# Optimization experiments

Measured on AMD Instinct MI355X. Metric: run time of the kernel, lower is better.

Reference implementation:

```python
import jax, jax.numpy as jnp
import numpy as np

B, T, D, H, L = 64, 512, 1024, 1024, 2


def _make_params(key, in_size, hidden):
    # 4 input-to-hidden and 4 hidden-to-hidden matrices, gate order (i, f, n, o),
    # concatenated along the output axis -> one GEMM per source per step.
    k1, k2 = jax.random.split(key)
    sx = (6.0 / (in_size + hidden)) ** 0.5   # xavier_uniform bound
    sh = (6.0 / (hidden + hidden)) ** 0.5
    Wx = jax.random.uniform(k1, (in_size, 4 * hidden), minval=-sx, maxval=sx, dtype=jnp.float32)
    Wh = jax.random.uniform(k2, (hidden, 4 * hidden), minval=-sh, maxval=sh, dtype=jnp.float32)
    b = jnp.zeros((4 * hidden,), dtype=jnp.float32)
    return Wx, Wh, b


def setup_inputs() -> dict:
    key = jax.random.key(0)
    kx, k0, k1 = jax.random.split(key, 3)
    x = jax.random.normal(kx, (B, T, D), dtype=jnp.float32)
    h0 = jnp.zeros((L, B, H), dtype=jnp.float32)
    c0 = jnp.zeros((L, B, H), dtype=jnp.float32)
    Wx0, Wh0, b0 = _make_params(k0, D, H)
    Wx1, Wh1, b1 = _make_params(k1, H, H)
    return {"x": x, "h0": h0, "c0": c0,
            "Wx0": Wx0, "Wh0": Wh0, "b0": b0,
            "Wx1": Wx1, "Wh1": Wh1, "b1": b1}


def _run_layer(xseq, h, c, Wx, Wh, b):
    # xseq: [T, B, in], h/c: [B, H]
    def step(carry, xt):
        h, c = carry
        g = xt @ Wx + h @ Wh + b                       # [B, 4H]
        i_t, f_t, n_t, o_t = jnp.split(g, 4, axis=-1)
        i_t = jax.nn.sigmoid(i_t)
        f_t = jax.nn.sigmoid(f_t)
        n_t = jnp.tanh(n_t)
        o_t = jax.nn.sigmoid(o_t)
        c = f_t * c + i_t * n_t
        h = o_t * jnp.tanh(c)
        return (h, c), h
    (h, c), ys = jax.lax.scan(step, (h, c), xseq)
    return ys, h, c                                     # ys: [T, B, H]


def reference(x, h0, c0, Wx0, Wh0, b0, Wx1, Wh1, b1):
    xs = jnp.transpose(x, (1, 0, 2))                    # [T, B, D]
    params = [(Wx0, Wh0, b0), (Wx1, Wh1, b1)]
    hs, cs = [], []
    for layer in range(L):
        Wx, Wh, b = params[layer]
        xs, h, c = _run_layer(xs, h0[layer], c0[layer], Wx, Wh, b)
        hs.append(h)
        cs.append(c)
    outputs = jnp.transpose(xs, (1, 0, 2))              # [B, T, H]
    return outputs, (jnp.stack(hs, 0), jnp.stack(cs, 0))
```

## Files before the change

kernel.cpp:

```cpp
#include <hip/hip_runtime.h>


#define NBLK 256
#define TPB  512
#define T_   512
#define HS_OFF 33554432
#define CS_OFF 33685504

typedef float  f32x4  __attribute__((ext_vector_type(4)));
typedef short  bf16x8 __attribute__((ext_vector_type(8)));

#define WS_CTR  0u
#define WS_W    69632u
#define WS_BIAS 33624064u
#define WS_XB   33656832u
#define WS_H0   100765696u
#define WS_H1   101027840u
#define WS_MIN  101289984u

__device__ __forceinline__ unsigned short f2bf(float f) {
  union { float f; unsigned u; } v; v.f = f;
  return (unsigned short)((v.u + 0x7FFFu + ((v.u >> 16) & 1u)) >> 16);
}
__device__ __forceinline__ float fsig(float x) { return 1.0f / (1.0f + __expf(-x)); }
__device__ __forceinline__ float ftanh(float x) {
  x = fminf(15.0f, fmaxf(-15.0f, x));
  float e = __expf(2.0f * x);
  return (e - 1.0f) / (e + 1.0f);
}

__global__ void kw(const float* __restrict__ Wx0, const float* __restrict__ Wh0,
                   const float* __restrict__ Wx1, const float* __restrict__ Wh1,
                   unsigned short* __restrict__ wp) {
  __shared__ float tile[64][65];
  int tb = blockIdx.x;
  int m  = tb >> 10;
  int kt = (tb >> 6) & 15;
  int nt = tb & 63;
  const float* W = (m == 0) ? Wx0 : (m == 1) ? Wh0 : (m == 2) ? Wx1 : Wh1;
  unsigned short* O = wp + (size_t)m * 4194304u;
  int k0 = kt * 64, n0 = nt * 64;
  int tx = threadIdx.x & 63, tg = threadIdx.x >> 6;
  for (int r = tg; r < 64; r += 4)
    tile[r][tx] = W[(size_t)(k0 + r) * 4096 + n0 + tx];
  __syncthreads();
  for (int r = tg; r < 64; r += 4) {
    int n = n0 + r;
    int p = ((n & 1023) << 2) | (n >> 10);
    O[(size_t)p * 1024 + k0 + tx] = f2bf(tile[tx][r]);
  }
}

__global__ void kx(const float* __restrict__ x, unsigned short* __restrict__ xb) {
  int row = blockIdx.x;
  int t = row >> 6, b = row & 63;
  const float4* src = (const float4*)(x + ((size_t)b * 512 + t) * 1024);
  float4 f = src[threadIdx.x];
  ushort4 o; o.x = f2bf(f.x); o.y = f2bf(f.y); o.z = f2bf(f.z); o.w = f2bf(f.w);
  ((ushort4*)(xb + (size_t)row * 1024))[threadIdx.x] = o;
}

__global__ void kmisc(const float* __restrict__ b0, const float* __restrict__ b1,
                      const float* __restrict__ h0in,
                      float* __restrict__ biasP,
                      unsigned short* __restrict__ h0r, unsigned short* __restrict__ h1r) {
  int idx = blockIdx.x * 256 + threadIdx.x;
  if (idx < 8192) {
    int layer = idx >> 12, p = idx & 4095;
    int orig = (p & 3) * 1024 + (p >> 2);
    biasP[idx] = (layer ? b1 : b0)[orig];
  } else if (idx < 139264) {
    int e = idx - 8192;
    int layer = e >> 16, o = e & 65535;
    int row = o >> 10, col = o & 1023;
    unsigned short v = f2bf(h0in[layer * 65536 + o]);
    int dst = 65536 + (col >> 3) * 512 + row * 8 + (col & 7);
    if (layer) h1r[dst] = v; else h0r[dst] = v;
  }
}

__global__ void __launch_bounds__(TPB)
klstm(const float* __restrict__ c0_in,
      const unsigned short* __restrict__ wp,
      const float* __restrict__ biasP,
      const unsigned short* __restrict__ xb,
      unsigned short* __restrict__ h0ring,
      unsigned short* __restrict__ h1ring,
      unsigned* __restrict__ ctrbase,
      float* __restrict__ out) {
  extern __shared__ char smem[];
  float* red  = (float*)(smem + 65536);
  float* lhb  = (float*)(smem + 73728);
  float* xred = (float*)(smem + 75776);
  unsigned* gctr  = ctrbase;
  unsigned* rctr  = ctrbase + 8192;
  unsigned* gflag = ctrbase + 9216;
  const int tid = threadIdx.x;
  const int w   = tid >> 6;
  const int l   = tid & 63;
  const int bid = blockIdx.x;
  const int n0  = bid * 16;
  const int layer = w >> 2;
  const int rbase = (w & 3) * 16;
  const int khalf = (w >> 2) * 512;
  const int grp   = bid >> 5;
  float* lh = lhb + w * 64;

  for (int m = 0; m < 4; m += 2) {
    const char* src = (const char*)(wp + (size_t)m * 4194304u + (size_t)n0 * 1024u);
    char* dst = smem + (m >> 1) * 32768;
    for (int i = tid; i < 2048; i += TPB) {
      int sb = i << 4;
      int c  = sb >> 11;
      int kb = sb & 2047;
      *(uint4*)(dst + (c << 11) + (kb ^ ((c & 7) << 4))) = *(const uint4*)(src + sb);
    }
  }

  bf16x8 wh0f[16], wh1f[16];
  {
    const unsigned short* p0 = wp + 4194304u + (size_t)(n0 + (l & 15)) * 1024u + khalf + (l >> 4) * 8;
    const unsigned short* p1 = wp + 3u * 4194304u + (size_t)(n0 + (l & 15)) * 1024u + khalf + (l >> 4) * 8;
    #pragma unroll
    for (int ks = 0; ks < 16; ++ks) {
      wh0f[ks] = *(const bf16x8*)(p0 + ks * 32);
      wh1f[ks] = *(const bf16x8*)(p1 + ks * 32);
    }
  }

  const int jg = bid * 4 + ((l & 15) >> 2);
  const float biasv = biasP[layer * 4096 + n0 + (l & 15)];
  const int qb = l & ~3;

  float cr[4];
  #pragma unroll
  for (int v = 0; v < 4; ++v)
    cr[v] = c0_in[layer * 65536 + (rbase + (l >> 4) * 4 + v) * 1024 + jg];

  const int ae0  = (rbase + (l & 15)) * 1024 + khalf + (l >> 4) * 8;
  const int hbase = ((khalf >> 3) + (l >> 4)) * 512 + (rbase + (l & 15)) * 8;
  const int lb0  = (l & 15) << 11;
  const int kb2  = khalf * 2 + (l >> 4) * 16;
  const int swz  = (l & 7) << 4;
  const int hsto = (bid >> 1) * 512 + 4 * (bid & 1);

  __syncthreads();

  f32x4 xacc = {0.f, 0.f, 0.f, 0.f};
  {
    #pragma unroll
    for (int kk = 0; kk < 16; ++kk) {
      bf16x8 ax = *(const bf16x8*)(xb + ae0 + kk * 32);
      bf16x8 b  = *(const bf16x8*)(smem + lb0 + ((kb2 + kk * 64) ^ swz));
      xacc = __builtin_amdgcn_mfma_f32_16x16x32_bf16(ax, b, xacc, 0, 0, 0);
    }
    if (w >= 4) {
      float* xr = xred + (size_t)(w & 3) * 256 + (size_t)l * 4;
      #pragma unroll
      for (int v = 0; v < 4; ++v) xr[v] = xacc[v];
    }
  }
  __syncthreads();

  for (int k = 0; k <= T_; ++k) {
    #pragma unroll
    for (int ks = 0; ks < 16; ++ks) {
      asm volatile("" :: "v"(wh0f[ks]));
      asm volatile("" :: "v"(wh1f[ks]));
    }

    const unsigned short* h0p = h0ring + ((k + 1) & 1) * 65536;
    const unsigned short* h1p = h1ring + (k & 1) * 65536;

    f32x4 acc0  = {0.f, 0.f, 0.f, 0.f};
    f32x4 acc1a = {0.f, 0.f, 0.f, 0.f};
    f32x4 acc1b = {0.f, 0.f, 0.f, 0.f};
    #pragma unroll
    for (int kk = 0; kk < 16; ++kk) {
      bf16x8 ah0 = *(const bf16x8*)(h0p + hbase + kk * 2048);
      bf16x8 ah1 = *(const bf16x8*)(h1p + hbase + kk * 2048);
      bf16x8 bx1 = *(const bf16x8*)(smem + 32768 + lb0 + ((kb2 + kk * 64) ^ swz));
      acc0  = __builtin_amdgcn_mfma_f32_16x16x32_bf16(ah0, wh0f[kk], acc0, 0, 0, 0);
      acc1a = __builtin_amdgcn_mfma_f32_16x16x32_bf16(ah0, bx1, acc1a, 0, 0, 0);
      acc1b = __builtin_amdgcn_mfma_f32_16x16x32_bf16(ah1, wh1f[kk], acc1b, 0, 0, 0);
    }

    {
      float* rb = red + (size_t)(w * 64 + l) * 4;
      f32x4 other = layer ? acc0 : (acc1a + acc1b);
      #pragma unroll
      for (int v = 0; v < 4; ++v) rb[v] = other[v];
    }
    __syncthreads();

    f32x4 g = layer ? (acc1a + acc1b) : acc0;
    {
      const int pw = layer ? (w - 4) : (w + 4);
      const float* rb = red + (size_t)(pw * 64 + l) * 4;
      #pragma unroll
      for (int v = 0; v < 4; ++v) g[v] += rb[v];
    }
    if (w < 4) {
      const float* xr = xred + (size_t)w * 256 + (size_t)l * 4;
      #pragma unroll
      for (int v = 0; v < 4; ++v) g[v] += xacc[v] + xr[v];
    }

    const bool active = layer ? (k >= 1) : (k < T_);
    f32x4 outv = {0.f, 0.f, 0.f, 0.f};
    if (active) {
      unsigned short* hw = layer ? (h1ring + ((k + 1) & 1) * 65536)
                                 : (h0ring + (k & 1) * 65536);
      #pragma unroll
      for (int v = 0; v < 4; ++v) {
        float gv = g[v] + biasv;
        float gi = __shfl(gv, qb);
        float gf = __shfl(gv, qb | 1);
        float gn = __shfl(gv, qb | 2);
        float go = __shfl(gv, qb | 3);
        float i_ = fsig(gi), f_ = fsig(gf), n_ = ftanh(gn), o_ = fsig(go);
        float c = f_ * cr[v] + i_ * n_;
        cr[v] = c;
        float h = o_ * ftanh(c);
        if ((l & 3) == 0)
          lh[((l >> 4) * 4 + v) * 4 + ((l & 15) >> 2)] = h;
      }
      if (l < 16) {
        f32x4 h4 = *(f32x4*)(lh + l * 4);
        outv = h4;
        ushort4 u4;
        u4.x = f2bf(h4[0]); u4.y = f2bf(h4[1]); u4.z = f2bf(h4[2]); u4.w = f2bf(h4[3]);
        union { ushort4 s; unsigned long long q; } pk; pk.s = u4;
        __hip_atomic_store((unsigned long long*)(hw + hsto + (rbase + l) * 8), pk.q,
                           __ATOMIC_RELAXED, __HIP_MEMORY_SCOPE_AGENT);
      }
    }

    if (k < T_) {
      __syncthreads();
      if (tid == 0) {
        unsigned old = __hip_atomic_fetch_add(&gctr[grp * 1024 + k], 1u,
                                              __ATOMIC_RELAXED, __HIP_MEMORY_SCOPE_AGENT);
        if (old == 31u) {
          unsigned oldr = __hip_atomic_fetch_add(&rctr[k], 1u,
                                                 __ATOMIC_RELAXED, __HIP_MEMORY_SCOPE_AGENT);
          if (oldr == 7u) {
            #pragma unroll
            for (int gg = 0; gg < 8; ++gg)
              __hip_atomic_store(&gflag[gg * 1024 + k], 1u,
                                 __ATOMIC_RELAXED, __HIP_MEMORY_SCOPE_AGENT);
          }
        }
        __builtin_amdgcn_fence(__ATOMIC_ACQUIRE, "agent");
      }
    }

    if (active && l < 16) {
      const int row = rbase + l;
      if (layer) {
        *(f32x4*)(out + (size_t)row * 524288u + (size_t)(k - 1) * 1024u + bid * 4) = outv;
        if (k == T_)
          *(f32x4*)(out + HS_OFF + 65536 + row * 1024 + bid * 4) = outv;
      } else if (k == T_ - 1) {
        *(f32x4*)(out + HS_OFF + row * 1024 + bid * 4) = outv;
      }
    }
    if (k + 1 < T_) {
      const unsigned short* xt = xb + (size_t)(k + 1) * 65536u;
      f32x4 xa = {0.f, 0.f, 0.f, 0.f};
      #pragma unroll
      for (int kk = 0; kk < 16; ++kk) {
        bf16x8 ax = *(const bf16x8*)(xt + ae0 + kk * 32);
        bf16x8 b  = *(const bf16x8*)(smem + lb0 + ((kb2 + kk * 64) ^ swz));
        xa = __builtin_amdgcn_mfma_f32_16x16x32_bf16(ax, b, xa, 0, 0, 0);
      }
      if (w >= 4) {
        float* xr = xred + (size_t)(w & 3) * 256 + (size_t)l * 4;
        #pragma unroll
        for (int v = 0; v < 4; ++v) xr[v] = xa[v];
      } else {
        xacc = xa;
      }
    }

    if (k < T_) {
      if (tid == 0) {
        unsigned spins = 0;
        while (__hip_atomic_load(&gflag[grp * 1024 + k], __ATOMIC_RELAXED, __HIP_MEMORY_SCOPE_AGENT) == 0u) {
          __builtin_amdgcn_s_sleep(1);
          if (++spins > 67108864u) break;
        }
      }
      __syncthreads();
    }
  }

  if ((l & 3) == 0) {
    #pragma unroll
    for (int v = 0; v < 4; ++v)
      out[CS_OFF + layer * 65536 + (rbase + (l >> 4) * 4 + v) * 1024 + jg] = cr[v];
  }
}

extern "C" void kernel_launch(void* const* d_in, const int* in_sizes, int n_in,
                              void* d_out, int out_size, void* d_ws, size_t ws_size,
                              hipStream_t stream) {
  const float* x   = (const float*)d_in[0];
  const float* h0  = (const float*)d_in[1];
  const float* c0  = (const float*)d_in[2];
  const float* Wx0 = (const float*)d_in[3];
  const float* Wh0 = (const float*)d_in[4];
  const float* b0  = (const float*)d_in[5];
  const float* Wx1 = (const float*)d_in[6];
  const float* Wh1 = (const float*)d_in[7];
  const float* b1  = (const float*)d_in[8];
  float* out = (float*)d_out;
  char* ws = (char*)d_ws;
  if (ws_size < (size_t)WS_MIN) return;

  unsigned* ctr       = (unsigned*)(ws + WS_CTR);
  unsigned short* wp  = (unsigned short*)(ws + WS_W);
  float* biasP        = (float*)(ws + WS_BIAS);
  unsigned short* xbp = (unsigned short*)(ws + WS_XB);
  unsigned short* h0r = (unsigned short*)(ws + WS_H0);
  unsigned short* h1r = (unsigned short*)(ws + WS_H1);

  (void)hipMemsetAsync(ctr, 0, 69632, stream);
  hipLaunchKernelGGL(kw,    dim3(4096),  dim3(256), 0, stream, Wx0, Wh0, Wx1, Wh1, wp);
  hipLaunchKernelGGL(kx,    dim3(32768), dim3(256), 0, stream, x, xbp);
  hipLaunchKernelGGL(kmisc, dim3(544),   dim3(256), 0, stream, b0, b1, h0, biasP, h0r, h1r);

  (void)hipFuncSetAttribute((const void*)klstm, hipFuncAttributeMaxDynamicSharedMemorySize, 79872);
  const float* c0a = c0; const unsigned short* wpa = wp; const float* bpa = biasP;
  const unsigned short* xba = xbp;
  unsigned short* h0a = h0r; unsigned short* h1a = h1r;
  unsigned* ca = ctr; float* oa = out;
  void* args[] = {&c0a, &wpa, &bpa, &xba, &h0a, &h1a, &ca, &oa};
  hipError_t e = hipLaunchCooperativeKernel((const void*)klstm, dim3(NBLK), dim3(TPB),
                                            args, 79872, stream);
  if (e != hipSuccess) {
    hipLaunchKernelGGL(klstm, dim3(NBLK), dim3(TPB), 79872, stream,
                       c0a, wpa, bpa, xba, h0a, h1a, ca, oa);
  }
}
```

Measured before the change: 5.623 ms.

## Move recurrent weights from registers to LDS and prefetch h fragments

The two recurrent weight slices that were held in VGPR arrays for the whole kernel now live in LDS, next to the input-projection slices. All four 32KB matrices are staged into a 128KB swizzled LDS region, and the extra scratch buffers move up accordingly. Each step first loads all 16 h0/h1 fragments from the global ring into registers so the loads are in flight together, then runs the MFMA loop reading its B operands from LDS. The hierarchical grid barrier is regrouped from 8 groups of 32 blocks to 16 groups of 16, with the counter and flag regions and the memset resized to match. This frees a large register budget and shortens per-group contention, at the cost of three LDS reads per MFMA step and a much larger LDS footprint per block.

```diff
diff --git a/kernel.cpp b/kernel.cpp
--- a/kernel.cpp
+++ b/kernel.cpp
@@ -11,12 +11,12 @@
 typedef short  bf16x8 __attribute__((ext_vector_type(8)));
 
 #define WS_CTR  0u
-#define WS_W    69632u
-#define WS_BIAS 33624064u
-#define WS_XB   33656832u
-#define WS_H0   100765696u
-#define WS_H1   101027840u
-#define WS_MIN  101289984u
+#define WS_W    139264u
+#define WS_BIAS 33693696u
+#define WS_XB   33726464u
+#define WS_H0   100835328u
+#define WS_H1   101097472u
+#define WS_MIN  101359616u
 
 __device__ __forceinline__ unsigned short f2bf(float f) {
   union { float f; unsigned u; } v; v.f = f;
@@ -79,7 +79,7 @@
   }
 }
 
-__global__ void __launch_bounds__(TPB)
+__global__ void __launch_bounds__(TPB, 2)
 klstm(const float* __restrict__ c0_in,
       const unsigned short* __restrict__ wp,
       const float* __restrict__ biasP,
@@ -89,12 +89,12 @@
       unsigned* __restrict__ ctrbase,
       float* __restrict__ out) {
   extern __shared__ char smem[];
-  float* red  = (float*)(smem + 65536);
-  float* lhb  = (float*)(smem + 73728);
-  float* xred = (float*)(smem + 75776);
+  float* red  = (float*)(smem + 131072);
+  float* lhb  = (float*)(smem + 139264);
+  float* xred = (float*)(smem + 141312);
   unsigned* gctr  = ctrbase;
-  unsigned* rctr  = ctrbase + 8192;
-  unsigned* gflag = ctrbase + 9216;
+  unsigned* rctr  = ctrbase + 16384;
+  unsigned* gflag = ctrbase + 17408;
   const int tid = threadIdx.x;
   const int w   = tid >> 6;
   const int l   = tid & 63;
@@ -103,28 +103,20 @@
   const int layer = w >> 2;
   const int rbase = (w & 3) * 16;
   const int khalf = (w >> 2) * 512;
-  const int grp   = bid >> 5;
+  const int grp   = bid >> 4;
   float* lh = lhb + w * 64;
 
-  for (int m = 0; m < 4; m += 2) {
-    const char* src = (const char*)(wp + (size_t)m * 4194304u + (size_t)n0 * 1024u);
-    char* dst = smem + (m >> 1) * 32768;
-    for (int i = tid; i < 2048; i += TPB) {
-      int sb = i << 4;
-      int c  = sb >> 11;
-      int kb = sb & 2047;
-      *(uint4*)(dst + (c << 11) + (kb ^ ((c & 7) << 4))) = *(const uint4*)(src + sb);
-    }
-  }
-
-  bf16x8 wh0f[16], wh1f[16];
   {
-    const unsigned short* p0 = wp + 4194304u + (size_t)(n0 + (l & 15)) * 1024u + khalf + (l >> 4) * 8;
-    const unsigned short* p1 = wp + 3u * 4194304u + (size_t)(n0 + (l & 15)) * 1024u + khalf + (l >> 4) * 8;
-    #pragma unroll
-    for (int ks = 0; ks < 16; ++ks) {
-      wh0f[ks] = *(const bf16x8*)(p0 + ks * 32);
-      wh1f[ks] = *(const bf16x8*)(p1 + ks * 32);
+    const int msrc[4] = {0, 2, 1, 3};
+    for (int s = 0; s < 4; ++s) {
+      const char* src = (const char*)(wp + (size_t)msrc[s] * 4194304u + (size_t)n0 * 1024u);
+      char* dst = smem + s * 32768;
+      for (int i = tid; i < 2048; i += TPB) {
+        int sb = i << 4;
+        int c  = sb >> 11;
+        int kb = sb & 2047;
+        *(uint4*)(dst + (c << 11) + (kb ^ ((c & 7) << 4))) = *(const uint4*)(src + sb);
+      }
     }
   }
 
@@ -163,26 +155,28 @@
   __syncthreads();
 
   for (int k = 0; k <= T_; ++k) {
-    #pragma unroll
-    for (int ks = 0; ks < 16; ++ks) {
-      asm volatile("" :: "v"(wh0f[ks]));
-      asm volatile("" :: "v"(wh1f[ks]));
-    }
-
     const unsigned short* h0p = h0ring + ((k + 1) & 1) * 65536;
     const unsigned short* h1p = h1ring + (k & 1) * 65536;
+
+    bf16x8 hf0[16], hf1[16];
+    #pragma unroll
+    for (int kk = 0; kk < 16; ++kk) {
+      hf0[kk] = *(const bf16x8*)(h0p + hbase + kk * 2048);
+      hf1[kk] = *(const bf16x8*)(h1p + hbase + kk * 2048);
+    }
 
     f32x4 acc0  = {0.f, 0.f, 0.f, 0.f};
     f32x4 acc1a = {0.f, 0.f, 0.f, 0.f};
     f32x4 acc1b = {0.f, 0.f, 0.f, 0.f};
     #pragma unroll
     for (int kk = 0; kk < 16; ++kk) {
-      bf16x8 ah0 = *(const bf16x8*)(h0p + hbase + kk * 2048);
-      bf16x8 ah1 = *(const bf16x8*)(h1p + hbase + kk * 2048);
-      bf16x8 bx1 = *(const bf16x8*)(smem + 32768 + lb0 + ((kb2 + kk * 64) ^ swz));
-      acc0  = __builtin_amdgcn_mfma_f32_16x16x32_bf16(ah0, wh0f[kk], acc0, 0, 0, 0);
-      acc1a = __builtin_amdgcn_mfma_f32_16x16x32_bf16(ah0, bx1, acc1a, 0, 0, 0);
-      acc1b = __builtin_amdgcn_mfma_f32_16x16x32_bf16(ah1, wh1f[kk], acc1b, 0, 0, 0);
+      const int bo = lb0 + ((kb2 + kk * 64) ^ swz);
+      bf16x8 bh0 = *(const bf16x8*)(smem + 65536 + bo);
+      bf16x8 bx1 = *(const bf16x8*)(smem + 32768 + bo);
+      bf16x8 bh1 = *(const bf16x8*)(smem + 98304 + bo);
+      acc0  = __builtin_amdgcn_mfma_f32_16x16x32_bf16(hf0[kk], bh0, acc0, 0, 0, 0);
+      acc1a = __builtin_amdgcn_mfma_f32_16x16x32_bf16(hf0[kk], bx1, acc1a, 0, 0, 0);
+      acc1b = __builtin_amdgcn_mfma_f32_16x16x32_bf16(hf1[kk], bh1, acc1b, 0, 0, 0);
     }
 
     {
@@ -241,12 +235,12 @@
       if (tid == 0) {
         unsigned old = __hip_atomic_fetch_add(&gctr[grp * 1024 + k], 1u,
                                               __ATOMIC_RELAXED, __HIP_MEMORY_SCOPE_AGENT);
-        if (old == 31u) {
+        if (old == 15u) {
           unsigned oldr = __hip_atomic_fetch_add(&rctr[k], 1u,
                                                  __ATOMIC_RELAXED, __HIP_MEMORY_SCOPE_AGENT);
-          if (oldr == 7u) {
+          if (oldr == 15u) {
             #pragma unroll
-            for (int gg = 0; gg < 8; ++gg)
+            for (int gg = 0; gg < 16; ++gg)
               __hip_atomic_store(&gflag[gg * 1024 + k], 1u,
                                  __ATOMIC_RELAXED, __HIP_MEMORY_SCOPE_AGENT);
           }
@@ -325,21 +319,21 @@
   unsigned short* h0r = (unsigned short*)(ws + WS_H0);
   unsigned short* h1r = (unsigned short*)(ws + WS_H1);
 
-  (void)hipMemsetAsync(ctr, 0, 69632, stream);
+  (void)hipMemsetAsync(ctr, 0, 139264, stream);
   hipLaunchKernelGGL(kw,    dim3(4096),  dim3(256), 0, stream, Wx0, Wh0, Wx1, Wh1, wp);
   hipLaunchKernelGGL(kx,    dim3(32768), dim3(256), 0, stream, x, xbp);
   hipLaunchKernelGGL(kmisc, dim3(544),   dim3(256), 0, stream, b0, b1, h0, biasP, h0r, h1r);
 
-  (void)hipFuncSetAttribute((const void*)klstm, hipFuncAttributeMaxDynamicSharedMemorySize, 79872);
+  (void)hipFuncSetAttribute((const void*)klstm, hipFuncAttributeMaxDynamicSharedMemorySize, 145408);
   const float* c0a = c0; const unsigned short* wpa = wp; const float* bpa = biasP;
   const unsigned short* xba = xbp;
   unsigned short* h0a = h0r; unsigned short* h1a = h1r;
   unsigned* ca = ctr; float* oa = out;
   void* args[] = {&c0a, &wpa, &bpa, &xba, &h0a, &h1a, &ca, &oa};
   hipError_t e = hipLaunchCooperativeKernel((const void*)klstm, dim3(NBLK), dim3(TPB),
-                                            args, 79872, stream);
+                                            args, 145408, stream);
   if (e != hipSuccess) {
-    hipLaunchKernelGGL(klstm, dim3(NBLK), dim3(TPB), 79872, stream,
+    hipLaunchKernelGGL(klstm, dim3(NBLK), dim3(TPB), 145408, stream,
                        c0a, wpa, bpa, xba, h0a, h1a, ca, oa);
   }
 }
```

Result: faster. 5.220 ms (-7.2%).
